# Kernel optimization log

Hardware: AMD Instinct MI355X
Metric: run time of the kernel (lower is better)

## Reference

```python
import jax, jax.numpy as jnp
import numpy as np

N_NODES = 50000
N_EDGES = 800000
C_IN = 64
C_HID = 64


def setup_inputs() -> dict:
    key = jax.random.key(0)
    k1, k2, k3, k4, k5 = jax.random.split(key, 5)
    x = jax.random.normal(k1, (N_NODES, C_IN), dtype=jnp.float32)
    edge_index = jax.random.randint(k2, (2, N_EDGES), 0, N_NODES, dtype=jnp.int64)
    edge_attr = jax.random.uniform(k3, (N_EDGES, 1), dtype=jnp.float32)
    # SplineConv params: kernel weight (K=1 collapsed), root weight, bias
    W = jax.random.normal(k4, (C_IN, C_HID), dtype=jnp.float32) * (1.0 / np.sqrt(C_IN))
    root = jax.random.normal(k5, (C_IN, C_HID), dtype=jnp.float32) * (1.0 / np.sqrt(C_IN))
    bias = jnp.zeros((C_HID,), dtype=jnp.float32)
    return {"x": x, "edge_index": edge_index, "edge_attr": edge_attr,
            "W": W, "root": root, "bias": bias}


def reference(x, edge_index, edge_attr, W, root, bias):
    # SplineConv(dim=1, kernel_size=1): the B-spline basis weights sum to 1
    # over the single kernel, so message_j = x_j @ W exactly (edge_attr drops out).
    src = edge_index[0]  # source nodes j
    dst = edge_index[1]  # target nodes i
    n = x.shape[0]
    h = x @ W                                   # [N, H] transform once per node
    msg_sum = jax.ops.segment_sum(h[src], dst, num_segments=n)   # scatter-add [N, H]
    deg = jax.ops.segment_sum(jnp.ones_like(dst, dtype=h.dtype), dst, num_segments=n)
    agg = msg_sum / jnp.clip(deg, 1.0)[:, None]  # mean aggregation
    out = agg + x @ root + bias                  # root weight + bias
    return jax.nn.relu(out)
```

## Files before the change

### kernel.cpp

```cpp
#include <hip/hip_runtime.h>

#define N_NODES 50000
#define N_EDGES 800000
#define C 64
#define BUCKET_NODES 256
#define NBUCK ((N_NODES + BUCKET_NODES - 1) / BUCKET_NODES)
#define BUCKET_CAP 6144
#define BIN_CHUNK 8192
#define NBIN_BLOCKS ((N_EDGES + BIN_CHUNK - 1) / BIN_CHUNK)
#define PREP_XBLOCKS 199
#define PB_BLOCKS (1 + PREP_XBLOCKS + NBIN_BLOCKS)
#define AGG_NODES 16
#define NAGG (N_NODES / AGG_NODES)
#define LDSTR 72

typedef __attribute__((ext_vector_type(8))) short bf16x8;
typedef __attribute__((ext_vector_type(4))) float f32x4;

__device__ inline unsigned short f2bf(float f) {
    union { float f; unsigned u; } v; v.f = f;
    unsigned r = v.u + 0x7FFF + ((v.u >> 16) & 1);
    return (unsigned short)(r >> 16);
}
__device__ inline float bf2f(unsigned short h) {
    union { unsigned u; float f; } v; v.u = (unsigned)h << 16;
    return v.f;
}

__global__ __launch_bounds__(256) void zero_cursor(int* __restrict__ c)
{
    c[threadIdx.x] = 0;
}

__global__ __launch_bounds__(256) void prep_bin(
    const float* __restrict__ x,
    const float* __restrict__ W,
    const float* __restrict__ R,
    const int*   __restrict__ ei,
    unsigned short* __restrict__ xbf,
    uint4* __restrict__ wpack,
    int* __restrict__ bucketCursor,
    int* __restrict__ bucketbuf)
{
    const int bid = blockIdx.x;

    if (bid == 0) {
        for (int s = threadIdx.x; s < 1024; s += 256) {
            const int f    = s >> 6;
            const int lane = s & 63;
            const int mat  = f >> 3, ks = (f >> 2) & 1, ct = f & 3;
            const float* src = mat ? R : W;
            const int kbase = ks * 32 + (lane >> 4) * 8;
            const int col   = ct * 16 + (lane & 15);
            unsigned wd[4];
            #pragma unroll
            for (int jj = 0; jj < 4; ++jj) {
                const unsigned lo16 = f2bf(src[(kbase + 2*jj    ) * C + col]);
                const unsigned hi16 = f2bf(src[(kbase + 2*jj + 1) * C + col]);
                wd[jj] = lo16 | (hi16 << 16);
            }
            uint4 o; o.x = wd[0]; o.y = wd[1]; o.z = wd[2]; o.w = wd[3];
            wpack[s] = o;
        }
        return;
    }

    if (bid <= PREP_XBLOCKS) {
        const int nthreads = PREP_XBLOCKS * 256;
        const int total4 = (N_NODES * C) / 4;
        for (int i = (bid - 1) * 256 + threadIdx.x; i < total4; i += nthreads) {
            const float4 v = ((const float4*)x)[i];
            ushort4 o;
            o.x = f2bf(v.x); o.y = f2bf(v.y); o.z = f2bf(v.z); o.w = f2bf(v.w);
            ((ushort4*)xbf)[i] = o;
        }
        return;
    }

    __shared__ int sdst[BIN_CHUNK];
    __shared__ int cnt[NBUCK], cnt2[NBUCK], gb[NBUCK];
    for (int i = threadIdx.x; i < NBUCK; i += 256) { cnt[i] = 0; cnt2[i] = 0; }
    __syncthreads();

    const int bb = bid - 1 - PREP_XBLOCKS;
    const int e0 = bb * BIN_CHUNK;
    const int e1 = min(e0 + BIN_CHUNK, N_EDGES);
    const int ne = e1 - e0;

    for (int k = threadIdx.x; k < ne; k += 256) {
        const int d = ei[N_EDGES + e0 + k];
        sdst[k] = d;
        atomicAdd(&cnt[((unsigned)d) >> 8], 1);
    }
    __syncthreads();

    for (int i = threadIdx.x; i < NBUCK; i += 256)
        gb[i] = atomicAdd(&bucketCursor[i], cnt[i]);
    __syncthreads();

    for (int k = threadIdx.x; k < ne; k += 256) {
        const int src = ei[e0 + k];
        const int dst = sdst[k];
        const int bkt = ((unsigned)dst) >> 8;
        const int off = gb[bkt] + atomicAdd(&cnt2[bkt], 1);
        bucketbuf[bkt * BUCKET_CAP + off] = (src << 8) | (dst & 255);
    }
}

__global__ __launch_bounds__(256) void csr_place_scan(
    const int* __restrict__ bucketCursor,
    const int* __restrict__ bucketbuf,
    int* __restrict__ rowptr,
    int* __restrict__ ebuf)
{
    __shared__ int entries[BUCKET_CAP];
    __shared__ int lcur[BUCKET_NODES];
    __shared__ int wsum[4];
    __shared__ int boffS;

    const int b    = blockIdx.x;
    const int tid  = threadIdx.x;
    const int lane = tid & 63, w = tid >> 6;
    const int lo   = b * BUCKET_NODES;
    const int nn   = min(BUCKET_NODES, N_NODES - lo);
    const int cnt  = bucketCursor[b];

    if (w == 0) {
        const int base = lane * 4;
        int s0 = (base+0 < NBUCK) ? bucketCursor[base+0] : 0;
        int s1 = (base+1 < NBUCK) ? bucketCursor[base+1] : 0;
        int s2 = (base+2 < NBUCK) ? bucketCursor[base+2] : 0;
        int s3 = (base+3 < NBUCK) ? bucketCursor[base+3] : 0;
        const int tot = s0 + s1 + s2 + s3;
        int incl = tot;
        #pragma unroll
        for (int off = 1; off < 64; off <<= 1) {
            const int t = __shfl_up(incl, off);
            if (lane >= off) incl += t;
        }
        if (lane == (b >> 2)) {
            int v = incl - tot;
            if ((b & 3) > 0) v += s0;
            if ((b & 3) > 1) v += s1;
            if ((b & 3) > 2) v += s2;
            boffS = v;
        }
    }

    lcur[tid] = 0;
    for (int k = tid; k < cnt; k += 256) entries[k] = bucketbuf[b * BUCKET_CAP + k];
    __syncthreads();

    for (int k = tid; k < cnt; k += 256)
        atomicAdd(&lcur[entries[k] & 255], 1);
    __syncthreads();

    const int v = (tid < nn) ? lcur[tid] : 0;
    int incl = v;
    #pragma unroll
    for (int off = 1; off < 64; off <<= 1) {
        const int t = __shfl_up(incl, off);
        if (lane >= off) incl += t;
    }
    if (lane == 63) wsum[w] = incl;
    __syncthreads();
    int woff = boffS;
    for (int k = 0; k < 4; ++k) if (k < w) woff += wsum[k];
    const int excl = woff + incl - v;
    __syncthreads();
    if (tid < nn) {
        rowptr[lo + tid] = excl;
        lcur[tid] = excl;
        if (lo + tid == N_NODES - 1) rowptr[N_NODES] = excl + v;
    }
    __syncthreads();

    for (int k = tid; k < cnt; k += 256) {
        const int p   = entries[k];
        const int pos = atomicAdd(&lcur[p & 255], 1);
        ebuf[pos] = p >> 8;
    }
}

__global__ __launch_bounds__(256) void agg_mfma(
    const int* __restrict__ rowptr,
    const int* __restrict__ ebuf,
    const unsigned short* __restrict__ xbf,
    const uint4*  __restrict__ wpack,
    const float*  __restrict__ bias,
    float* __restrict__ out)
{
    __shared__ unsigned short aggs[AGG_NODES][LDSTR];

    const int lane = threadIdx.x & 63;
    const int w    = threadIdx.x >> 6;
    const int tileBase = (int)blockIdx.x * AGG_NODES;

    const int r = lane & 15;
    const int g = lane >> 4;

    #pragma unroll
    for (int i = 0; i < 4; ++i) {
        const int n   = tileBase + w * 4 + i;
        const int beg = rowptr[n];
        const int end = rowptr[n + 1];
        float a0 = 0.f, a1 = 0.f, a2 = 0.f, a3 = 0.f;
        for (int base = beg; base < end; base += 64) {
            const int m = min(64, end - base);
            const int sid = (base + lane < end) ? ebuf[base + lane] : 0;
            for (int j = 0; j < m; j += 4) {
                const int  e     = j + g;
                const bool valid = e < m;
                const int  s     = __shfl(sid, valid ? e : 0);
                const uint2 v = *(const uint2*)(xbf + (size_t)s * C + r * 4);
                if (valid) {
                    a0 += bf2f((unsigned short)(v.x & 0xffff));
                    a1 += bf2f((unsigned short)(v.x >> 16));
                    a2 += bf2f((unsigned short)(v.y & 0xffff));
                    a3 += bf2f((unsigned short)(v.y >> 16));
                }
            }
        }
        #pragma unroll
        for (int off = 16; off <= 32; off <<= 1) {
            a0 += __shfl_xor(a0, off);
            a1 += __shfl_xor(a1, off);
            a2 += __shfl_xor(a2, off);
            a3 += __shfl_xor(a3, off);
        }
        if (g == 0) {
            const float inv = 1.0f / fmaxf((float)(end - beg), 1.0f);
            uint2 pv;
            pv.x = (unsigned)f2bf(a0 * inv) | ((unsigned)f2bf(a1 * inv) << 16);
            pv.y = (unsigned)f2bf(a2 * inv) | ((unsigned)f2bf(a3 * inv) << 16);
            *(uint2*)&aggs[w * 4 + i][r * 4] = pv;
        }
    }
    __syncthreads();

    const int q = lane >> 4;

    const bf16x8 bw0 = *(const bf16x8*)&wpack[(0*8 + 0*4 + w) * 64 + lane];
    const bf16x8 bw1 = *(const bf16x8*)&wpack[(0*8 + 1*4 + w) * 64 + lane];
    const bf16x8 br0 = *(const bf16x8*)&wpack[(1*8 + 0*4 + w) * 64 + lane];
    const bf16x8 br1 = *(const bf16x8*)&wpack[(1*8 + 1*4 + w) * 64 + lane];
    const float  bb  = bias[w * 16 + r];

    const unsigned short* rx = xbf + (size_t)(tileBase + r) * C;
    const bf16x8 a0 = *(const bf16x8*)&aggs[r][q * 8];
    const bf16x8 a1 = *(const bf16x8*)&aggs[r][32 + q * 8];
    const bf16x8 a2 = *(const bf16x8*)(rx + q * 8);
    const bf16x8 a3 = *(const bf16x8*)(rx + 32 + q * 8);

    f32x4 acc4 = {0.f, 0.f, 0.f, 0.f};
    acc4 = __builtin_amdgcn_mfma_f32_16x16x32_bf16(a0, bw0, acc4, 0, 0, 0);
    acc4 = __builtin_amdgcn_mfma_f32_16x16x32_bf16(a1, bw1, acc4, 0, 0, 0);
    acc4 = __builtin_amdgcn_mfma_f32_16x16x32_bf16(a2, br0, acc4, 0, 0, 0);
    acc4 = __builtin_amdgcn_mfma_f32_16x16x32_bf16(a3, br1, acc4, 0, 0, 0);

    #pragma unroll
    for (int i = 0; i < 4; ++i) {
        const int node = tileBase + q * 4 + i;
        out[(size_t)node * C + w * 16 + r] = fmaxf(acc4[i] + bb, 0.f);
    }
}

extern "C" void kernel_launch(void* const* d_in, const int* in_sizes, int n_in,
                              void* d_out, int out_size, void* d_ws, size_t ws_size,
                              hipStream_t stream)
{
    const float* x    = (const float*)d_in[0];
    const int*   ei   = (const int*)d_in[1];
    const float* W    = (const float*)d_in[3];
    const float* R    = (const float*)d_in[4];
    const float* bias = (const float*)d_in[5];

    char* wsb = (char*)d_ws;
    unsigned short* xbf = (unsigned short*)wsb;
    size_t off = (size_t)N_NODES * C * sizeof(unsigned short);
    uint4* wpack        = (uint4*)(wsb + off);  off += 1024 * sizeof(uint4);
    int*   bucketCursor = (int*)(wsb + off);    off += 256 * sizeof(int);
    int*   rowptr       = (int*)(wsb + off);    off += ((N_NODES + 8) & ~3) * sizeof(int);
    int*   ebuf         = (int*)(wsb + off);    off += (size_t)N_EDGES * sizeof(int);
    int*   bucketbuf    = (int*)(wsb + off);
    float* out          = (float*)d_out;

    zero_cursor   <<<1, 256, 0, stream>>>(bucketCursor);
    prep_bin      <<<PB_BLOCKS, 256, 0, stream>>>(x, W, R, ei, xbf, wpack,
                                                  bucketCursor, bucketbuf);
    csr_place_scan<<<NBUCK, 256, 0, stream>>>(bucketCursor, bucketbuf, rowptr, ebuf);
    agg_mfma      <<<NAGG, 256, 0, stream>>>(rowptr, ebuf, xbf, wpack, bias, out);
}
```

Measured before the change: 71.42 us.

## Replace global bucket atomics with per-block count grid and unroll gather loop

Binning blocks now write per-(bin,bucket) counts and fixed-capacity cells instead of atomically reserving space in global bucket cursors. This removes the zero_cursor launch and global atomics. The placement kernel reconstructs offsets by summing and scanning the count grid. The aggregation gather loop is unrolled to issue four independent row loads per step, raising memory-level parallelism. The cells cap at 104 entries, so a heavily skewed destination distribution would silently drop edges, and the compaction pass reads a larger padded region.

```diff
diff --git a/kernel.cpp b/kernel.cpp
--- a/kernel.cpp
+++ b/kernel.cpp
@@ -4,12 +4,14 @@
 #define N_EDGES 800000
 #define C 64
 #define BUCKET_NODES 256
-#define NBUCK ((N_NODES + BUCKET_NODES - 1) / BUCKET_NODES)
-#define BUCKET_CAP 6144
+#define NBUCK 196
 #define BIN_CHUNK 8192
-#define NBIN_BLOCKS ((N_EDGES + BIN_CHUNK - 1) / BIN_CHUNK)
-#define PREP_XBLOCKS 199
-#define PB_BLOCKS (1 + PREP_XBLOCKS + NBIN_BLOCKS)
+#define NBIN 98
+#define CAP_CELL 104
+#define ENT_CAP 6144
+#define GRID_A 512
+#define WPACK_BID 98
+#define XCONV0 99
 #define AGG_NODES 16
 #define NAGG (N_NODES / AGG_NODES)
 #define LDSTR 72
@@ -27,36 +29,59 @@
     return v.f;
 }
 
-__global__ __launch_bounds__(256) void zero_cursor(int* __restrict__ c)
-{
-    c[threadIdx.x] = 0;
-}
-
 __global__ __launch_bounds__(256) void prep_bin(
     const float* __restrict__ x,
-    const float* __restrict__ W,
-    const float* __restrict__ R,
     const int*   __restrict__ ei,
+    const float* __restrict__ Wm,
+    const float* __restrict__ Rm,
     unsigned short* __restrict__ xbf,
     uint4* __restrict__ wpack,
-    int* __restrict__ bucketCursor,
+    int* __restrict__ counts,
     int* __restrict__ bucketbuf)
 {
     const int bid = blockIdx.x;
-
-    if (bid == 0) {
-        for (int s = threadIdx.x; s < 1024; s += 256) {
-            const int f    = s >> 6;
-            const int lane = s & 63;
-            const int mat  = f >> 3, ks = (f >> 2) & 1, ct = f & 3;
-            const float* src = mat ? R : W;
-            const int kbase = ks * 32 + (lane >> 4) * 8;
-            const int col   = ct * 16 + (lane & 15);
+    const int tid = threadIdx.x;
+
+    if (bid < NBIN) {
+        __shared__ int sdst[BIN_CHUNK];
+        __shared__ int cnt[NBUCK], cnt2[NBUCK];
+        for (int i = tid; i < NBUCK; i += 256) { cnt[i] = 0; cnt2[i] = 0; }
+        __syncthreads();
+        const int e0 = bid * BIN_CHUNK;
+        const int ne = min(BIN_CHUNK, N_EDGES - e0);
+        for (int k = tid; k < ne; k += 256) {
+            const int d = ei[N_EDGES + e0 + k];
+            sdst[k] = d;
+            atomicAdd(&cnt[((unsigned)d) >> 8], 1);
+        }
+        __syncthreads();
+        for (int j = tid; j < NBUCK; j += 256)
+            counts[bid * NBUCK + j] = min(cnt[j], CAP_CELL);
+        for (int k = tid; k < ne; k += 256) {
+            const int src = ei[e0 + k];
+            const int d   = sdst[k];
+            const int j   = ((unsigned)d) >> 8;
+            const int s   = atomicAdd(&cnt2[j], 1);
+            if (s < CAP_CELL)
+                bucketbuf[((size_t)j * NBIN + bid) * CAP_CELL + s] =
+                    (src << 8) | (d & 255);
+        }
+        return;
+    }
+
+    if (bid == WPACK_BID) {
+        for (int s = tid; s < 1024; s += 256) {
+            const int f = s >> 6;
+            const int l = s & 63;
+            const int mat = f >> 3, ks = (f >> 2) & 1, ct = f & 3;
+            const float* srcm = mat ? Rm : Wm;
+            const int kbase = ks * 32 + (l >> 4) * 8;
+            const int col   = ct * 16 + (l & 15);
             unsigned wd[4];
             #pragma unroll
             for (int jj = 0; jj < 4; ++jj) {
-                const unsigned lo16 = f2bf(src[(kbase + 2*jj    ) * C + col]);
-                const unsigned hi16 = f2bf(src[(kbase + 2*jj + 1) * C + col]);
+                const unsigned lo16 = f2bf(srcm[(kbase + 2*jj    ) * C + col]);
+                const unsigned hi16 = f2bf(srcm[(kbase + 2*jj + 1) * C + col]);
                 wd[jj] = lo16 | (hi16 << 16);
             }
             uint4 o; o.x = wd[0]; o.y = wd[1]; o.z = wd[2]; o.w = wd[3];
@@ -65,56 +90,26 @@
         return;
     }
 
-    if (bid <= PREP_XBLOCKS) {
-        const int nthreads = PREP_XBLOCKS * 256;
-        const int total4 = (N_NODES * C) / 4;
-        for (int i = (bid - 1) * 256 + threadIdx.x; i < total4; i += nthreads) {
-            const float4 v = ((const float4*)x)[i];
-            ushort4 o;
-            o.x = f2bf(v.x); o.y = f2bf(v.y); o.z = f2bf(v.z); o.w = f2bf(v.w);
-            ((ushort4*)xbf)[i] = o;
-        }
-        return;
-    }
-
-    __shared__ int sdst[BIN_CHUNK];
-    __shared__ int cnt[NBUCK], cnt2[NBUCK], gb[NBUCK];
-    for (int i = threadIdx.x; i < NBUCK; i += 256) { cnt[i] = 0; cnt2[i] = 0; }
-    __syncthreads();
-
-    const int bb = bid - 1 - PREP_XBLOCKS;
-    const int e0 = bb * BIN_CHUNK;
-    const int e1 = min(e0 + BIN_CHUNK, N_EDGES);
-    const int ne = e1 - e0;
-
-    for (int k = threadIdx.x; k < ne; k += 256) {
-        const int d = ei[N_EDGES + e0 + k];
-        sdst[k] = d;
-        atomicAdd(&cnt[((unsigned)d) >> 8], 1);
-    }
-    __syncthreads();
-
-    for (int i = threadIdx.x; i < NBUCK; i += 256)
-        gb[i] = atomicAdd(&bucketCursor[i], cnt[i]);
-    __syncthreads();
-
-    for (int k = threadIdx.x; k < ne; k += 256) {
-        const int src = ei[e0 + k];
-        const int dst = sdst[k];
-        const int bkt = ((unsigned)dst) >> 8;
-        const int off = gb[bkt] + atomicAdd(&cnt2[bkt], 1);
-        bucketbuf[bkt * BUCKET_CAP + off] = (src << 8) | (dst & 255);
+    const int nthreads = (GRID_A - XCONV0) * 256;
+    const int total4 = (N_NODES * C) / 4;
+    for (int i = (bid - XCONV0) * 256 + tid; i < total4; i += nthreads) {
+        const float4 v = ((const float4*)x)[i];
+        ushort4 o;
+        o.x = f2bf(v.x); o.y = f2bf(v.y); o.z = f2bf(v.z); o.w = f2bf(v.w);
+        ((ushort4*)xbf)[i] = o;
     }
 }
 
 __global__ __launch_bounds__(256) void csr_place_scan(
-    const int* __restrict__ bucketCursor,
+    const int* __restrict__ counts,
     const int* __restrict__ bucketbuf,
     int* __restrict__ rowptr,
     int* __restrict__ ebuf)
 {
-    __shared__ int entries[BUCKET_CAP];
+    __shared__ int entries[ENT_CAP];
     __shared__ int lcur[BUCKET_NODES];
+    __shared__ int colsum[NBUCK];
+    __shared__ int cnts[NBIN], coff[NBIN];
     __shared__ int wsum[4];
     __shared__ int boffS;
 
@@ -123,14 +118,24 @@
     const int lane = tid & 63, w = tid >> 6;
     const int lo   = b * BUCKET_NODES;
     const int nn   = min(BUCKET_NODES, N_NODES - lo);
-    const int cnt  = bucketCursor[b];
+
+    if (tid < NBUCK) {
+        int s = 0;
+        for (int i = 0; i < NBIN; ++i) s += counts[i * NBUCK + tid];
+        colsum[tid] = s;
+    }
+    if (tid >= 256 - NBIN) {
+        const int i = tid - (256 - NBIN);
+        cnts[i] = counts[i * NBUCK + b];
+    }
+    __syncthreads();
 
     if (w == 0) {
         const int base = lane * 4;
-        int s0 = (base+0 < NBUCK) ? bucketCursor[base+0] : 0;
-        int s1 = (base+1 < NBUCK) ? bucketCursor[base+1] : 0;
-        int s2 = (base+2 < NBUCK) ? bucketCursor[base+2] : 0;
-        int s3 = (base+3 < NBUCK) ? bucketCursor[base+3] : 0;
+        int s0 = (base+0 < NBUCK) ? colsum[base+0] : 0;
+        int s1 = (base+1 < NBUCK) ? colsum[base+1] : 0;
+        int s2 = (base+2 < NBUCK) ? colsum[base+2] : 0;
+        int s3 = (base+3 < NBUCK) ? colsum[base+3] : 0;
         const int tot = s0 + s1 + s2 + s3;
         int incl = tot;
         #pragma unroll
@@ -145,10 +150,32 @@
             if ((b & 3) > 2) v += s2;
             boffS = v;
         }
-    }
-
+    } else if (w == 1) {
+        const int l2 = lane * 2;
+        const int c0 = (l2     < NBIN) ? cnts[l2]     : 0;
+        const int c1 = (l2 + 1 < NBIN) ? cnts[l2 + 1] : 0;
+        const int pair = c0 + c1;
+        int incl = pair;
+        #pragma unroll
+        for (int off = 1; off < 64; off <<= 1) {
+            const int t = __shfl_up(incl, off);
+            if (lane >= off) incl += t;
+        }
+        const int excl = incl - pair;
+        if (l2     < NBIN) coff[l2]     = excl;
+        if (l2 + 1 < NBIN) coff[l2 + 1] = excl + c0;
+    }
     lcur[tid] = 0;
-    for (int k = tid; k < cnt; k += 256) entries[k] = bucketbuf[b * BUCKET_CAP + k];
+    __syncthreads();
+
+    const int cnt = colsum[b];
+    const int* mybuf = bucketbuf + (size_t)b * NBIN * CAP_CELL;
+    for (int k = tid; k < NBIN * CAP_CELL; k += 256) {
+        const int i = k / CAP_CELL;
+        const int s = k - i * CAP_CELL;
+        if (s < cnts[i])
+            entries[coff[i] + s] = mybuf[(size_t)i * CAP_CELL + s];
+    }
     __syncthreads();
 
     for (int k = tid; k < cnt; k += 256)
@@ -165,7 +192,7 @@
     if (lane == 63) wsum[w] = incl;
     __syncthreads();
     int woff = boffS;
-    for (int k = 0; k < 4; ++k) if (k < w) woff += wsum[k];
+    for (int k2 = 0; k2 < 4; ++k2) if (k2 < w) woff += wsum[k2];
     const int excl = woff + incl - v;
     __syncthreads();
     if (tid < nn) {
@@ -208,7 +235,34 @@
         for (int base = beg; base < end; base += 64) {
             const int m = min(64, end - base);
             const int sid = (base + lane < end) ? ebuf[base + lane] : 0;
-            for (int j = 0; j < m; j += 4) {
+            int j = 0;
+            for (; j + 16 <= m; j += 16) {
+                const int s0 = __shfl(sid, j + g);
+                const int s1 = __shfl(sid, j + 4  + g);
+                const int s2 = __shfl(sid, j + 8  + g);
+                const int s3 = __shfl(sid, j + 12 + g);
+                const uint2 v0 = *(const uint2*)(xbf + (size_t)s0 * C + r * 4);
+                const uint2 v1 = *(const uint2*)(xbf + (size_t)s1 * C + r * 4);
+                const uint2 v2 = *(const uint2*)(xbf + (size_t)s2 * C + r * 4);
+                const uint2 v3 = *(const uint2*)(xbf + (size_t)s3 * C + r * 4);
+                a0 += bf2f((unsigned short)(v0.x & 0xffff)) +
+                      bf2f((unsigned short)(v1.x & 0xffff)) +
+                      bf2f((unsigned short)(v2.x & 0xffff)) +
+                      bf2f((unsigned short)(v3.x & 0xffff));
+                a1 += bf2f((unsigned short)(v0.x >> 16)) +
+                      bf2f((unsigned short)(v1.x >> 16)) +
+                      bf2f((unsigned short)(v2.x >> 16)) +
+                      bf2f((unsigned short)(v3.x >> 16));
+                a2 += bf2f((unsigned short)(v0.y & 0xffff)) +
+                      bf2f((unsigned short)(v1.y & 0xffff)) +
+                      bf2f((unsigned short)(v2.y & 0xffff)) +
+                      bf2f((unsigned short)(v3.y & 0xffff));
+                a3 += bf2f((unsigned short)(v0.y >> 16)) +
+                      bf2f((unsigned short)(v1.y >> 16)) +
+                      bf2f((unsigned short)(v2.y >> 16)) +
+                      bf2f((unsigned short)(v3.y >> 16));
+            }
+            for (; j < m; j += 4) {
                 const int  e     = j + g;
                 const bool valid = e < m;
                 const int  s     = __shfl(sid, valid ? e : 0);
@@ -278,16 +332,15 @@
     char* wsb = (char*)d_ws;
     unsigned short* xbf = (unsigned short*)wsb;
     size_t off = (size_t)N_NODES * C * sizeof(unsigned short);
-    uint4* wpack        = (uint4*)(wsb + off);  off += 1024 * sizeof(uint4);
-    int*   bucketCursor = (int*)(wsb + off);    off += 256 * sizeof(int);
-    int*   rowptr       = (int*)(wsb + off);    off += ((N_NODES + 8) & ~3) * sizeof(int);
-    int*   ebuf         = (int*)(wsb + off);    off += (size_t)N_EDGES * sizeof(int);
-    int*   bucketbuf    = (int*)(wsb + off);
-    float* out          = (float*)d_out;
-
-    zero_cursor   <<<1, 256, 0, stream>>>(bucketCursor);
-    prep_bin      <<<PB_BLOCKS, 256, 0, stream>>>(x, W, R, ei, xbf, wpack,
-                                                  bucketCursor, bucketbuf);
-    csr_place_scan<<<NBUCK, 256, 0, stream>>>(bucketCursor, bucketbuf, rowptr, ebuf);
+    uint4* wpack     = (uint4*)(wsb + off);  off += 1024 * sizeof(uint4);
+    int*   counts    = (int*)(wsb + off);    off += 19456 * sizeof(int);
+    int*   rowptr    = (int*)(wsb + off);    off += ((N_NODES + 8) & ~3) * sizeof(int);
+    int*   ebuf      = (int*)(wsb + off);    off += (size_t)N_EDGES * sizeof(int);
+    int*   bucketbuf = (int*)(wsb + off);
+    float* out       = (float*)d_out;
+
+    prep_bin      <<<GRID_A, 256, 0, stream>>>(x, ei, W, R, xbf, wpack,
+                                               counts, bucketbuf);
+    csr_place_scan<<<NBUCK, 256, 0, stream>>>(counts, bucketbuf, rowptr, ebuf);
     agg_mfma      <<<NAGG, 256, 0, stream>>>(rowptr, ebuf, xbf, wpack, bias, out);
 }
```

Result: slower. 76.47 us (+7.1%).
